# Kernel optimization log

Measured on AMD Instinct MI355X. Metric: run time of the kernel, lower is better.

## Reference

```python
import jax, jax.numpy as jnp
import numpy as np

N_NODES = 50000
N_EDGES = 400000
D = 64          # in/out channels (residual forces equality)
H = 8           # attention heads
L = 3           # number of GATv2 layers
NEG_SLOPE = 0.2
LN_EPS = 1e-5


def setup_inputs() -> dict:
    key = jax.random.key(0)
    ks = jax.random.split(key, 6)
    x = jax.random.normal(ks[0], (N_NODES, D), dtype=jnp.float32)
    edge_index = jax.random.randint(ks[1], (2, N_EDGES), 0, N_NODES, dtype=jnp.int64)
    scale = 1.0 / np.sqrt(D)
    Wl = jax.random.normal(ks[2], (L, D, H * D), dtype=jnp.float32) * scale
    Wr = jax.random.normal(ks[3], (L, D, H * D), dtype=jnp.float32) * scale
    att = jax.random.normal(ks[4], (L, H, D), dtype=jnp.float32) * 0.1
    b = jnp.zeros((L, D), dtype=jnp.float32)
    gamma = jnp.ones((L, D), dtype=jnp.float32)
    beta = jnp.zeros((L, D), dtype=jnp.float32)
    return {"x": x, "Wl": Wl, "Wr": Wr, "att": att, "b": b,
            "gamma": gamma, "beta": beta, "edge_index": edge_index}


def _gatv2_stack(x, Wl, Wr, att, b, gamma, beta, src, dst, num_nodes):
    # src/dst already include self-loops (PyG add_self_loops=True)
    for l in range(Wl.shape[0]):
        xl = (x @ Wl[l]).reshape(num_nodes, H, -1)   # [N,H,C] messages (source transform)
        xr = (x @ Wr[l]).reshape(num_nodes, H, -1)   # [N,H,C] target transform
        m = jax.nn.leaky_relu(xl[src] + xr[dst], NEG_SLOPE)       # [E,H,C]
        e = jnp.einsum('ehc,hc->eh', m, att[l])                    # [E,H]
        # segment softmax over incoming edges of each target node
        emax = jax.ops.segment_max(e, dst, num_segments=num_nodes)
        ex = jnp.exp(e - emax[dst])
        denom = jax.ops.segment_sum(ex, dst, num_segments=num_nodes)
        alpha = ex / denom[dst]                                    # [E,H]
        agg = jax.ops.segment_sum(alpha[:, :, None] * xl[src], dst,
                                  num_segments=num_nodes)          # [N,H,C]
        h = agg.mean(axis=1) + b[l]                                # concat=False -> head mean, + bias
        x = h + x                                                  # residual
        mu = x.mean(-1, keepdims=True)
        var = x.var(-1, keepdims=True)
        x = (x - mu) / jnp.sqrt(var + LN_EPS) * gamma[l] + beta[l] # LayerNorm
        x = jax.nn.relu(x)
    return x


def reference(x, Wl, Wr, att, b, gamma, beta, edge_index):
    num_nodes = x.shape[0]
    loops = jnp.arange(num_nodes, dtype=edge_index.dtype)
    src = jnp.concatenate([edge_index[0], loops])
    dst = jnp.concatenate([edge_index[1], loops])
    return _gatv2_stack(x, Wl, Wr, att, b, gamma, beta, src, dst, num_nodes)
```

## Files before the change

kernel.cpp:

```cpp
#include <hip/hip_runtime.h>

#define N_NODES 50000
#define N_EDGES 400000
#define EP (N_EDGES + N_NODES)
#define D 64
#define H 8
#define NEG_SLOPE 0.2f
#define LN_EPS 1e-5f
#define CHUNK 196
#define SCAN_BLOCKS 256
#define PAD_N 50048

typedef unsigned short ushort_t;
typedef unsigned int uint_t;
typedef __attribute__((ext_vector_type(8))) short short8;
typedef __attribute__((ext_vector_type(4))) float f32x4;
typedef __attribute__((ext_vector_type(2))) float f32x2;

__device__ __forceinline__ ushort_t f2bf(float f) {
    uint_t u = __float_as_uint(f);
    u += 0x7fffu + ((u >> 16) & 1u);
    return (ushort_t)(u >> 16);
}
__device__ __forceinline__ f32x2 mkf2(uint_t u) {
    f32x2 r;
    r.x = __uint_as_float(u << 16);
    r.y = __uint_as_float(u & 0xffff0000u);
    return r;
}
__device__ __forceinline__ f32x2 absf2(f32x2 a) {
    f32x2 r;
    r.x = __uint_as_float(__float_as_uint(a.x) & 0x7fffffffu);
    r.y = __uint_as_float(__float_as_uint(a.y) & 0x7fffffffu);
    return r;
}

__device__ __forceinline__ void edge_sd(const int* __restrict__ ei, int eid, int& s, int& d) {
    if (eid < N_EDGES) { s = ei[eid]; d = ei[N_EDGES + eid]; }
    else               { s = d = eid - N_EDGES; }
}


__global__ __launch_bounds__(256) void setup_all(const int* __restrict__ ei, int* __restrict__ counts,
                                                 const float* __restrict__ x,
                                                 const float* __restrict__ Wl, const float* __restrict__ Wr,
                                                 ushort_t* __restrict__ xb, ushort_t* __restrict__ Wt) {
    int t = blockIdx.x * 256 + threadIdx.x;
    if (t < EP) {
        int s, d; edge_sd(ei, t, s, d);
        atomicAdd(&counts[d], 1);
        return;
    }
    t -= EP;
    if (t < N_NODES * 64) { xb[t] = f2bf(x[t]); return; }
    t -= N_NODES * 64;
    if (t >= 3 * 1024 * 64) return;
    int l = t >> 16, rem = t & 65535, col = rem >> 6, k = rem & 63;
    float v = (col < 512) ? Wl[((size_t)l * 64 + k) * 512 + col]
                          : Wr[((size_t)l * 64 + k) * 512 + (col - 512)];
    Wt[t] = f2bf(v);
}


__global__ __launch_bounds__(256) void csr_scan1(const int* __restrict__ counts, int* __restrict__ bsum) {
    __shared__ int sd[256];
    int t = threadIdx.x, b = blockIdx.x;
    int idx = b * CHUNK + t;
    sd[t] = (t < CHUNK && idx < N_NODES) ? counts[idx] : 0;
    __syncthreads();
    for (int d = 128; d > 0; d >>= 1) {
        if (t < d) sd[t] += sd[t + d];
        __syncthreads();
    }
    if (t == 0) bsum[b] = sd[0];
}

__global__ __launch_bounds__(256) void csr_scan2(int* __restrict__ bsum) {
    __shared__ int sd[256];
    int t = threadIdx.x;
    sd[t] = bsum[t];
    __syncthreads();
    for (int d = 1; d < 256; d <<= 1) {
        int v = (t >= d) ? sd[t - d] : 0;
        __syncthreads();
        if (t >= d) sd[t] += v;
        __syncthreads();
    }
    bsum[t] = (t > 0) ? sd[t - 1] : 0;
}

__global__ __launch_bounds__(256) void csr_scan3(const int* __restrict__ counts, const int* __restrict__ bsum,
                                                 int* __restrict__ offsets, int* __restrict__ cursor,
                                                 int* __restrict__ bhist) {
    __shared__ int sd[256];
    __shared__ int hist[64];
    int t = threadIdx.x, b = blockIdx.x;
    if (t < 64) hist[t] = 0;
    int idx = b * CHUNK + t;
    int v = (t < CHUNK && idx < N_NODES) ? counts[idx] : 0;
    sd[t] = v;
    __syncthreads();
    for (int d = 1; d < 256; d <<= 1) {
        int u = (t >= d) ? sd[t - d] : 0;
        __syncthreads();
        if (t >= d) sd[t] += u;
        __syncthreads();
    }
    if (t < CHUNK && idx < N_NODES) {
        int ex = bsum[b] + sd[t] - v;
        offsets[idx] = ex;
        cursor[idx]  = ex;
        atomicAdd(&hist[63 - min(v, 63)], 1);
    }
    __syncthreads();
    if (t < 64) bhist[b * 64 + t] = hist[t];
    if (b == 0 && t == 0) offsets[N_NODES] = EP;
}

__global__ void deg_scan(const int* __restrict__ bhist, int* __restrict__ pbase) {
    __shared__ int tot[64], base[64];
    int t = threadIdx.x;
    if (t < 64) {
        int s = 0;
        for (int b = 0; b < SCAN_BLOCKS; ++b) s += bhist[b * 64 + t];
        tot[t] = s;
    }
    __syncthreads();
    if (t == 0) {
        int run = 0;
        for (int k = 0; k < 64; ++k) { base[k] = run; run += tot[k]; }
    }
    __syncthreads();
    if (t < 64) {
        int run = base[t];
        for (int b = 0; b < SCAN_BLOCKS; ++b) { pbase[b * 64 + t] = run; run += bhist[b * 64 + t]; }
    }
}

__global__ __launch_bounds__(256) void deg_place(const int* __restrict__ counts, const int* __restrict__ pbase,
                                                 int* __restrict__ node_order) {
    __shared__ int cur[64];
    int t = threadIdx.x, b = blockIdx.x;
    if (t < 64) cur[t] = pbase[b * 64 + t];
    __syncthreads();
    int idx = b * CHUNK + t;
    if (t < CHUNK && idx < N_NODES) {
        int bin = 63 - min(counts[idx], 63);
        int p = atomicAdd(&cur[bin], 1);
        node_order[p] = idx;
    }
}

__global__ __launch_bounds__(256) void csr_scatter(const int* __restrict__ ei, int* __restrict__ cursor,
                                                   int* __restrict__ csr_src) {
    int t = blockIdx.x * 256 + threadIdx.x;
    if (t >= EP) return;
    int s, d; edge_sd(ei, t, s, d);
    int pos = atomicAdd(&cursor[d], 1);
    csr_src[pos] = s;
}

__global__ __launch_bounds__(256) void gemm_mfma(const ushort_t* __restrict__ xb,
                                                 const ushort_t* __restrict__ Wt,
                                                 ushort_t* __restrict__ xlr) {
    __shared__ ushort_t sW[128 * 72];
    int t = threadIdx.x;
    int colq = blockIdx.y;
    const ushort_t* Wg = Wt + (size_t)colq * 128 * 64;
    {
        int col = t >> 1, half = t & 1;
        const uint4* g = (const uint4*)(Wg + col * 64 + half * 32);
        uint4* l = (uint4*)(sW + col * 72 + half * 32);
        l[0] = g[0]; l[1] = g[1]; l[2] = g[2]; l[3] = g[3];
    }
    __syncthreads();
    int lane = t & 63, w = t >> 6;
    int ln = lane & 15, q = lane >> 4;
    int node = blockIdx.x * 64 + w * 16 + ln;
    int nclamp = node < N_NODES ? node : N_NODES - 1;
    const short8 b0 = *(const short8*)(xb + (size_t)nclamp * 64 + q * 8);
    const short8 b1 = *(const short8*)(xb + (size_t)nclamp * 64 + 32 + q * 8);
#pragma unroll
    for (int ct = 0; ct < 8; ++ct) {
        const short8 a0 = *(const short8*)(sW + (ct * 16 + ln) * 72 + q * 8);
        const short8 a1 = *(const short8*)(sW + (ct * 16 + ln) * 72 + 32 + q * 8);
        f32x4 acc = {0.f, 0.f, 0.f, 0.f};
        acc = __builtin_amdgcn_mfma_f32_16x16x32_bf16(a0, b0, acc, 0, 0, 0);
        acc = __builtin_amdgcn_mfma_f32_16x16x32_bf16(a1, b1, acc, 0, 0, 0);
        if (node < N_NODES) {
            uint_t lo = (uint_t)f2bf(acc[0]) | ((uint_t)f2bf(acc[1]) << 16);
            uint_t hi = (uint_t)f2bf(acc[2]) | ((uint_t)f2bf(acc[3]) << 16);
            *(uint2*)(xlr + (size_t)node * 1024 + colq * 128 + ct * 16 + q * 4) = make_uint2(lo, hi);
        }
    }
}

__global__ __launch_bounds__(256) void node_fused(const float* __restrict__ x_in,
                                                  const ushort_t* __restrict__ xlr,
                                                  const float* __restrict__ att,
                                                  const int* __restrict__ offsets, const int* __restrict__ csr_src,
                                                  const int* __restrict__ node_order,
                                                  const float* __restrict__ bias, const float* __restrict__ gamma,
                                                  const float* __restrict__ beta, float* __restrict__ x_out,
                                                  ushort_t* __restrict__ xb_out) {
    int n = node_order[blockIdx.x * 4 + (threadIdx.x >> 6)];
    n = __builtin_amdgcn_readfirstlane(n);
    int lane = threadIdx.x & 63;
    int h = lane >> 3, i = lane & 7;
    int beg = __builtin_amdgcn_readfirstlane(offsets[n]);
    int end = __builtin_amdgcn_readfirstlane(offsets[n + 1]);
    int off = h * 64 + i * 8;

    uint4 ru = *(const uint4*)(xlr + (size_t)n * 1024 + 512 + off);
    f32x2 rv0 = mkf2(ru.x), rv1 = mkf2(ru.y), rv2 = mkf2(ru.z), rv3 = mkf2(ru.w);
    const float4* pa = (const float4*)(att + h * 64 + i * 8);
    float4 aa = pa[0], ab = pa[1];
    f32x2 a0 = {aa.x, aa.y}, a1 = {aa.z, aa.w}, a2 = {ab.x, ab.y}, a3 = {ab.z, ab.w};
    f32x2 a60 = 0.6f * a0, a61 = 0.6f * a1, a62 = 0.6f * a2, a63 = 0.6f * a3;
    f32x2 a40 = 0.4f * a0, a41 = 0.4f * a1, a42 = 0.4f * a2, a43 = 0.4f * a3;
    float par = 0.6f * (a0.x * rv0.x + a0.y * rv0.y + a1.x * rv1.x + a1.y * rv1.y +
                        a2.x * rv2.x + a2.y * rv2.y + a3.x * rv3.x + a3.y * rv3.y);

    float den = 0.f;
    f32x2 acc0 = {0.f, 0.f}, acc1 = {0.f, 0.f}, acc2 = {0.f, 0.f}, acc3 = {0.f, 0.f};

#define PROCESS(cur)                                                     \
    {                                                                    \
        f32x2 v0 = mkf2(cur.x), v1 = mkf2(cur.y),                        \
              v2 = mkf2(cur.z), v3 = mkf2(cur.w);                        \
        f32x2 p = a60 * v0;                                              \
        p = a61 * v1 + p;                                                \
        p = a62 * v2 + p;                                                \
        p = a63 * v3 + p;                                                \
        p = a40 * absf2(v0 + rv0) + p;                                   \
        p = a41 * absf2(v1 + rv1) + p;                                   \
        p = a42 * absf2(v2 + rv2) + p;                                   \
        p = a43 * absf2(v3 + rv3) + p;                                   \
        float pdot = p.x + p.y + par;                                    \
        pdot += __shfl_xor(pdot, 1);                                     \
        pdot += __shfl_xor(pdot, 2);                                     \
        pdot += __shfl_xor(pdot, 4);                                     \
        float wgt = __expf(pdot);                                        \
        den += wgt;                                                      \
        f32x2 wv = {wgt, wgt};                                           \
        acc0 = wv * v0 + acc0;                                           \
        acc1 = wv * v1 + acc1;                                           \
        acc2 = wv * v2 + acc2;                                           \
        acc3 = wv * v3 + acc3;                                           \
    }

    for (int base = beg; base < end; base += 64) {
        int idx = base + lane;
        int srcs = csr_src[idx < end ? idx : end - 1];
        int cnt = min(64, end - base);
        int j = 0;
        for (; j + 8 <= cnt; j += 8) {
            uint4 q[8];
#pragma unroll
            for (int u = 0; u < 8; ++u) {
                int ss = __shfl(srcs, j + u);
                q[u] = *(const uint4*)(xlr + (size_t)ss * 1024 + off);
            }
#pragma unroll
            for (int u = 0; u < 8; ++u) PROCESS(q[u]);
        }
        for (; j < cnt; ++j) {
            int ss = __shfl(srcs, j);
            uint4 qq = *(const uint4*)(xlr + (size_t)ss * 1024 + off);
            PROCESS(qq);
        }
    }
#undef PROCESS

    float invden = 0.125f / den;
    f32x2 iv = {invden, invden};
    acc0 *= iv; acc1 *= iv; acc2 *= iv; acc3 *= iv;
    float acc[8] = {acc0.x, acc0.y, acc1.x, acc1.y, acc2.x, acc2.y, acc3.x, acc3.y};
#pragma unroll
    for (int dm = 8; dm < 64; dm <<= 1) {
#pragma unroll
        for (int k2 = 0; k2 < 8; ++k2) acc[k2] += __shfl_xor(acc[k2], dm);
    }

    int cbase = i * 8;
    const float4* px = (const float4*)(x_in + n * 64 + cbase);
    float4 x0 = px[0], x1 = px[1];
    float xi[8] = {x0.x, x0.y, x0.z, x0.w, x1.x, x1.y, x1.z, x1.w};
    float v[8];
    float sum = 0.f, sq = 0.f;
#pragma unroll
    for (int k2 = 0; k2 < 8; ++k2) {
        float val = acc[k2] + bias[cbase + k2] + xi[k2];
        v[k2] = val; sum += val; sq += val * val;
    }
#pragma unroll
    for (int dm = 1; dm < 8; dm <<= 1) { sum += __shfl_xor(sum, dm); sq += __shfl_xor(sq, dm); }
    float mu   = sum * (1.0f / 64.0f);
    float var  = sq * (1.0f / 64.0f) - mu * mu;
    float rstd = rsqrtf(var + LN_EPS);

    if (h == 0) {
        float o[8];
#pragma unroll
        for (int k2 = 0; k2 < 8; ++k2) {
            float y = (v[k2] - mu) * rstd * gamma[cbase + k2] + beta[cbase + k2];
            o[k2] = fmaxf(y, 0.f);
        }
        float4* po = (float4*)(x_out + n * 64 + cbase);
        po[0] = make_float4(o[0], o[1], o[2], o[3]);
        po[1] = make_float4(o[4], o[5], o[6], o[7]);
        uint_t w0 = (uint_t)f2bf(o[0]) | ((uint_t)f2bf(o[1]) << 16);
        uint_t w1 = (uint_t)f2bf(o[2]) | ((uint_t)f2bf(o[3]) << 16);
        uint_t w2 = (uint_t)f2bf(o[4]) | ((uint_t)f2bf(o[5]) << 16);
        uint_t w3 = (uint_t)f2bf(o[6]) | ((uint_t)f2bf(o[7]) << 16);
        *(uint4*)(xb_out + (size_t)n * 64 + cbase) = make_uint4(w0, w1, w2, w3);
    }
}


extern "C" void kernel_launch(void* const* d_in, const int* in_sizes, int n_in,
                              void* d_out, int out_size, void* d_ws, size_t ws_size,
                              hipStream_t stream) {
    const float* x     = (const float*)d_in[0];
    const float* Wl    = (const float*)d_in[1];
    const float* Wr    = (const float*)d_in[2];
    const float* att   = (const float*)d_in[3];
    const float* b     = (const float*)d_in[4];
    const float* gamma = (const float*)d_in[5];
    const float* beta  = (const float*)d_in[6];
    const int*   ei    = (const int*)d_in[7];
    float* out = (float*)d_out;

    ushort_t* xlr = (ushort_t*)d_ws;
    ushort_t* xb  = xlr + (size_t)N_NODES * 1024;
    ushort_t* Wt  = xb + (size_t)PAD_N * 64;
    int* counts     = (int*)(Wt + 3 * 1024 * 64);
    int* offsets    = counts + PAD_N;
    int* cursor     = offsets + PAD_N;
    int* bsum       = cursor + PAD_N;
    int* node_order = bsum + 256;
    int* bhist      = node_order + PAD_N;
    int* pbase      = bhist + SCAN_BLOCKS * 64;
    int* csr_src    = pbase + SCAN_BLOCKS * 64;

    hipMemsetAsync(counts, 0, N_NODES * sizeof(int), stream);

    int setup_threads = EP + N_NODES * 64 + 3 * 1024 * 64;
    setup_all<<<(setup_threads + 255) / 256, 256, 0, stream>>>(ei, counts, x, Wl, Wr, xb, Wt);

    csr_scan1 <<<SCAN_BLOCKS, 256, 0, stream>>>(counts, bsum);
    csr_scan2 <<<1, 256, 0, stream>>>(bsum);
    csr_scan3 <<<SCAN_BLOCKS, 256, 0, stream>>>(counts, bsum, offsets, cursor, bhist);
    deg_scan  <<<1, 256, 0, stream>>>(bhist, pbase);
    deg_place <<<SCAN_BLOCKS, 256, 0, stream>>>(counts, pbase, node_order);
    int eb = (EP + 255) / 256;
    csr_scatter<<<eb, 256, 0, stream>>>(ei, cursor, csr_src);

    const float* xin = x;
    dim3 ggrid(PAD_N / 64, 8);
    for (int l = 0; l < 3; ++l) {
        gemm_mfma <<<ggrid, 256, 0, stream>>>(xb, Wt + (size_t)l * 1024 * 64, xlr);
        node_fused<<<N_NODES / 4, 256, 0, stream>>>(xin, xlr, att + l * (H * D), offsets, csr_src,
                                                    node_order, b + l * D, gamma + l * D, beta + l * D,
                                                    out, xb);
        xin = out;
    }
}
```

Before: 477.3 us.

## Merge placement and scatter kernels, drop redundant logit term, use packed bf16 convert

```diff
diff --git a/kernel.cpp b/kernel.cpp
--- a/kernel.cpp
+++ b/kernel.cpp
@@ -17,10 +17,27 @@
 typedef __attribute__((ext_vector_type(4))) float f32x4;
 typedef __attribute__((ext_vector_type(2))) float f32x2;
 
+#if defined(__has_builtin)
+#if __has_builtin(__builtin_amdgcn_cvt_pk_bf16_f32)
+#define HAVE_CVT_PK_BF16 1
+#endif
+#endif
+
 __device__ __forceinline__ ushort_t f2bf(float f) {
     uint_t u = __float_as_uint(f);
     u += 0x7fffu + ((u >> 16) & 1u);
     return (ushort_t)(u >> 16);
+}
+__device__ __forceinline__ uint_t pack_bf2(float a, float b) {
+#ifdef HAVE_CVT_PK_BF16
+    typedef __attribute__((ext_vector_type(2))) __bf16 bf16x2_t;
+    bf16x2_t v = __builtin_amdgcn_cvt_pk_bf16_f32(a, b);
+    uint_t r;
+    __builtin_memcpy(&r, &v, 4);
+    return r;
+#else
+    return (uint_t)f2bf(a) | ((uint_t)f2bf(b) << 16);
+#endif
 }
 __device__ __forceinline__ f32x2 mkf2(uint_t u) {
     f32x2 r;
@@ -137,59 +154,54 @@
     }
 }
 
-__global__ __launch_bounds__(256) void deg_place(const int* __restrict__ counts, const int* __restrict__ pbase,
-                                                 int* __restrict__ node_order) {
-    __shared__ int cur[64];
-    int t = threadIdx.x, b = blockIdx.x;
-    if (t < 64) cur[t] = pbase[b * 64 + t];
-    __syncthreads();
-    int idx = b * CHUNK + t;
-    if (t < CHUNK && idx < N_NODES) {
-        int bin = 63 - min(counts[idx], 63);
-        int p = atomicAdd(&cur[bin], 1);
-        node_order[p] = idx;
-    }
-}
-
-__global__ __launch_bounds__(256) void csr_scatter(const int* __restrict__ ei, int* __restrict__ cursor,
-                                                   int* __restrict__ csr_src) {
-    int t = blockIdx.x * 256 + threadIdx.x;
-    if (t >= EP) return;
-    int s, d; edge_sd(ei, t, s, d);
-    int pos = atomicAdd(&cursor[d], 1);
-    csr_src[pos] = s;
+__global__ __launch_bounds__(256) void place_scatter(const int* __restrict__ counts, const int* __restrict__ pbase,
+                                                     int* __restrict__ node_order,
+                                                     const int* __restrict__ ei, int* __restrict__ cursor,
+                                                     int* __restrict__ csr_src) {
+    int b = blockIdx.x;
+    if (b < SCAN_BLOCKS) {
+        __shared__ int cur[64];
+        int t = threadIdx.x;
+        if (t < 64) cur[t] = pbase[b * 64 + t];
+        __syncthreads();
+        int idx = b * CHUNK + t;
+        if (t < CHUNK && idx < N_NODES) {
+            int bin = 63 - min(counts[idx], 63);
+            int p = atomicAdd(&cur[bin], 1);
+            node_order[p] = idx;
+        }
+    } else {
+        int t = (b - SCAN_BLOCKS) * 256 + threadIdx.x;
+        if (t >= EP) return;
+        int s, d; edge_sd(ei, t, s, d);
+        int pos = atomicAdd(&cursor[d], 1);
+        csr_src[pos] = s;
+    }
 }
 
 __global__ __launch_bounds__(256) void gemm_mfma(const ushort_t* __restrict__ xb,
                                                  const ushort_t* __restrict__ Wt,
                                                  ushort_t* __restrict__ xlr) {
-    __shared__ ushort_t sW[128 * 72];
     int t = threadIdx.x;
-    int colq = blockIdx.y;
-    const ushort_t* Wg = Wt + (size_t)colq * 128 * 64;
-    {
-        int col = t >> 1, half = t & 1;
-        const uint4* g = (const uint4*)(Wg + col * 64 + half * 32);
-        uint4* l = (uint4*)(sW + col * 72 + half * 32);
-        l[0] = g[0]; l[1] = g[1]; l[2] = g[2]; l[3] = g[3];
-    }
-    __syncthreads();
     int lane = t & 63, w = t >> 6;
     int ln = lane & 15, q = lane >> 4;
+    int colq = blockIdx.y;
     int node = blockIdx.x * 64 + w * 16 + ln;
     int nclamp = node < N_NODES ? node : N_NODES - 1;
     const short8 b0 = *(const short8*)(xb + (size_t)nclamp * 64 + q * 8);
     const short8 b1 = *(const short8*)(xb + (size_t)nclamp * 64 + 32 + q * 8);
+    const ushort_t* Wbase = Wt + (size_t)colq * 128 * 64;
 #pragma unroll
     for (int ct = 0; ct < 8; ++ct) {
-        const short8 a0 = *(const short8*)(sW + (ct * 16 + ln) * 72 + q * 8);
-        const short8 a1 = *(const short8*)(sW + (ct * 16 + ln) * 72 + 32 + q * 8);
+        int col = ct * 16 + ln;
+        const short8 a0 = *(const short8*)(Wbase + col * 64 + q * 8);
+        const short8 a1 = *(const short8*)(Wbase + col * 64 + 32 + q * 8);
         f32x4 acc = {0.f, 0.f, 0.f, 0.f};
         acc = __builtin_amdgcn_mfma_f32_16x16x32_bf16(a0, b0, acc, 0, 0, 0);
         acc = __builtin_amdgcn_mfma_f32_16x16x32_bf16(a1, b1, acc, 0, 0, 0);
         if (node < N_NODES) {
-            uint_t lo = (uint_t)f2bf(acc[0]) | ((uint_t)f2bf(acc[1]) << 16);
-            uint_t hi = (uint_t)f2bf(acc[2]) | ((uint_t)f2bf(acc[3]) << 16);
+            uint_t lo = pack_bf2(acc[0], acc[1]);
+            uint_t hi = pack_bf2(acc[2], acc[3]);
             *(uint2*)(xlr + (size_t)node * 1024 + colq * 128 + ct * 16 + q * 4) = make_uint2(lo, hi);
         }
     }
@@ -218,8 +230,6 @@
     f32x2 a0 = {aa.x, aa.y}, a1 = {aa.z, aa.w}, a2 = {ab.x, ab.y}, a3 = {ab.z, ab.w};
     f32x2 a60 = 0.6f * a0, a61 = 0.6f * a1, a62 = 0.6f * a2, a63 = 0.6f * a3;
     f32x2 a40 = 0.4f * a0, a41 = 0.4f * a1, a42 = 0.4f * a2, a43 = 0.4f * a3;
-    float par = 0.6f * (a0.x * rv0.x + a0.y * rv0.y + a1.x * rv1.x + a1.y * rv1.y +
-                        a2.x * rv2.x + a2.y * rv2.y + a3.x * rv3.x + a3.y * rv3.y);
 
     float den = 0.f;
     f32x2 acc0 = {0.f, 0.f}, acc1 = {0.f, 0.f}, acc2 = {0.f, 0.f}, acc3 = {0.f, 0.f};
@@ -236,7 +246,7 @@
         p = a41 * absf2(v1 + rv1) + p;                                   \
         p = a42 * absf2(v2 + rv2) + p;                                   \
         p = a43 * absf2(v3 + rv3) + p;                                   \
-        float pdot = p.x + p.y + par;                                    \
+        float pdot = p.x + p.y;                                          \
         pdot += __shfl_xor(pdot, 1);                                     \
         pdot += __shfl_xor(pdot, 2);                                     \
         pdot += __shfl_xor(pdot, 4);                                     \
@@ -309,11 +319,9 @@
         float4* po = (float4*)(x_out + n * 64 + cbase);
         po[0] = make_float4(o[0], o[1], o[2], o[3]);
         po[1] = make_float4(o[4], o[5], o[6], o[7]);
-        uint_t w0 = (uint_t)f2bf(o[0]) | ((uint_t)f2bf(o[1]) << 16);
-        uint_t w1 = (uint_t)f2bf(o[2]) | ((uint_t)f2bf(o[3]) << 16);
-        uint_t w2 = (uint_t)f2bf(o[4]) | ((uint_t)f2bf(o[5]) << 16);
-        uint_t w3 = (uint_t)f2bf(o[6]) | ((uint_t)f2bf(o[7]) << 16);
-        *(uint4*)(xb_out + (size_t)n * 64 + cbase) = make_uint4(w0, w1, w2, w3);
+        *(uint4*)(xb_out + (size_t)n * 64 + cbase) =
+            make_uint4(pack_bf2(o[0], o[1]), pack_bf2(o[2], o[3]),
+                       pack_bf2(o[4], o[5]), pack_bf2(o[6], o[7]));
     }
 }
 
@@ -348,13 +356,12 @@
     int setup_threads = EP + N_NODES * 64 + 3 * 1024 * 64;
     setup_all<<<(setup_threads + 255) / 256, 256, 0, stream>>>(ei, counts, x, Wl, Wr, xb, Wt);
 
-    csr_scan1 <<<SCAN_BLOCKS, 256, 0, stream>>>(counts, bsum);
-    csr_scan2 <<<1, 256, 0, stream>>>(bsum);
-    csr_scan3 <<<SCAN_BLOCKS, 256, 0, stream>>>(counts, bsum, offsets, cursor, bhist);
-    deg_scan  <<<1, 256, 0, stream>>>(bhist, pbase);
-    deg_place <<<SCAN_BLOCKS, 256, 0, stream>>>(counts, pbase, node_order);
+    csr_scan1<<<SCAN_BLOCKS, 256, 0, stream>>>(counts, bsum);
+    csr_scan2<<<1, 256, 0, stream>>>(bsum);
+    csr_scan3<<<SCAN_BLOCKS, 256, 0, stream>>>(counts, bsum, offsets, cursor, bhist);
+    deg_scan <<<1, 256, 0, stream>>>(bhist, pbase);
     int eb = (EP + 255) / 256;
-    csr_scatter<<<eb, 256, 0, stream>>>(ei, cursor, csr_src);
+    place_scatter<<<SCAN_BLOCKS + eb, 256, 0, stream>>>(counts, pbase, node_order, ei, cursor, csr_src);
 
     const float* xin = x;
     dim3 ggrid(PAD_N / 64, 8);
```

Result: slower. 547.5 us (+14.7%).
